# Kernel optimization log

Hardware: AMD Instinct MI355X
Metric: run time of the kernel (lower is better)

The kernel has to match this reference:

```python
import jax, jax.numpy as jnp
import numpy as np

B, U, L, H = 2048, 512, 32, 64  # batch, num_units, latent_dim, hidden


def setup_inputs() -> dict:
    key = jax.random.key(0)
    ks = jax.random.split(key, 17)
    s = 0.05  # weight scale
    inp = {
        "x": jax.random.normal(ks[0], (B, U), dtype=jnp.float32),
        # encoder: U -> 64 -> 64 -> 64 -> L
        "We1": jax.random.normal(ks[1], (U, H), jnp.float32) * s,
        "be1": jnp.zeros((H,), jnp.float32),
        "We2": jax.random.normal(ks[2], (H, H), jnp.float32) * s,
        "be2": jnp.zeros((H,), jnp.float32),
        "We3": jax.random.normal(ks[3], (H, H), jnp.float32) * s,
        "be3": jnp.zeros((H,), jnp.float32),
        "We4": jax.random.normal(ks[4], (H, L), jnp.float32) * s,
        "be4": jnp.zeros((L,), jnp.float32),
        # U disjoint decoders, weights stacked along unit axis: L -> 64 -> 64 -> 64 -> 1
        "Wd1": jax.random.normal(ks[5], (U, L, H), jnp.float32) * s,
        "bd1": jnp.zeros((U, H), jnp.float32),
        "Wd2": jax.random.normal(ks[6], (U, H, H), jnp.float32) * s,
        "bd2": jnp.zeros((U, H), jnp.float32),
        "Wd3": jax.random.normal(ks[7], (U, H, H), jnp.float32) * s,
        "bd3": jnp.zeros((U, H), jnp.float32),
        "Wd4": jax.random.normal(ks[8], (U, H), jnp.float32) * s,  # last layer out_dim=1, squeezed
        "bd4": jnp.zeros((U,), jnp.float32),
    }
    return inp


def reference(x, We1, be1, We2, be2, We3, be3, We4, be4,
              Wd1, bd1, Wd2, bd2, Wd3, bd3, Wd4, bd4):
    # shared encoder MLP: [B, U] -> [B, L]
    z = jax.nn.relu(x @ We1 + be1)
    z = jax.nn.relu(z @ We2 + be2)
    z = jax.nn.relu(z @ We3 + be3)
    z = z @ We4 + be4  # [B, L]
    # all U decoders batched as grouped GEMMs: [B, L] -> [B, U]
    h = jax.nn.relu(jnp.einsum('bl,ulh->buh', z, Wd1) + bd1)   # [B, U, H]
    h = jax.nn.relu(jnp.einsum('buh,uhk->buk', h, Wd2) + bd2)  # [B, U, H]
    h = jax.nn.relu(jnp.einsum('buh,uhk->buk', h, Wd3) + bd3)  # [B, U, H]
    out = jnp.einsum('buh,uh->bu', h, Wd4) + bd4               # [B, U]
    return out
```

## Files before the change

kernel.cpp:

```cpp
#include <hip/hip_runtime.h>
#include <hip/hip_bf16.h>
#include <hip/hip_fp16.h>
#include <stdint.h>

#define NB 2048
#define NU 512
#define NL 32
#define NH 64

typedef float    f4    __attribute__((ext_vector_type(4)));
typedef uint32_t u32x4 __attribute__((ext_vector_type(4)));
typedef _Float16 h8    __attribute__((ext_vector_type(8)));
typedef _Float16 h2    __attribute__((ext_vector_type(2)));

__device__ __forceinline__ f4 mfma16h(u32x4 a, u32x4 b, f4 c) {
    return __builtin_amdgcn_mfma_f32_16x16x32_f16(
        __builtin_bit_cast(h8, a), __builtin_bit_cast(h8, b), c, 0, 0, 0);
}

__device__ __forceinline__ uint32_t pk2h(float a, float b) {
    uint32_t la = (uint32_t)__half_as_ushort(__float2half_rn(a));
    uint32_t hb = (uint32_t)__half_as_ushort(__float2half_rn(b));
    return la | (hb << 16);
}

__device__ __forceinline__ uint32_t pk_rtz(float e, float o) {
    return __builtin_bit_cast(uint32_t, __builtin_amdgcn_cvt_pkrtz(e, o));
}

__device__ __forceinline__ uint32_t pk_relu(float e, float o) {
    uint32_t r = pk_rtz(e, o);
    asm("v_pk_max_f16 %0, %1, 0" : "=v"(r) : "v"(r));
    return r;
}

__device__ __forceinline__ float dot2(uint32_t a, uint32_t b, float c) {
    return __builtin_amdgcn_fdot2(__builtin_bit_cast(h2, a),
                                  __builtin_bit_cast(h2, b), c, false);
}

__device__ __forceinline__ void xch(uint32_t A, uint32_t B,
                                    uint32_t& o0, uint32_t& o1) {
    asm("v_permlane32_swap_b32 %0, %1" : "+v"(A), "+v"(B));
    asm("v_permlane16_swap_b32 %0, %1" : "+v"(A), "+v"(B));
    o0 = A; o1 = B;
}

__global__ __launch_bounds__(256)
void enc_kernel(const float* __restrict__ x,
                const float* __restrict__ We1, const float* __restrict__ be1,
                const float* __restrict__ We2, const float* __restrict__ be2,
                const float* __restrict__ We3, const float* __restrict__ be3,
                const float* __restrict__ We4, const float* __restrict__ be4,
                uint32_t* __restrict__ zpk)
{
    const int RE = 8;
    __shared__ float xs[RE][512];
    __shared__ float ws[128 * 64];
    __shared__ float h[RE][NH];
    __shared__ float h2s[RE][NH];

    const int t  = threadIdx.x;
    const int r0 = blockIdx.x * RE;

    {
        const f4* xv  = (const f4*)(x + (size_t)r0 * 512);
        f4*       xsv = (f4*)&xs[0][0];
        for (int i = t; i < RE * 512 / 4; i += 256) xsv[i] = xv[i];
    }

    const int j = t & 63;
    const int w = t >> 6;

    float acc0 = be1[j], acc1 = be1[j];
    for (int kc = 0; kc < 512; kc += 128) {
        __syncthreads();
        const f4* wv  = (const f4*)(We1 + (size_t)kc * 64);
        f4*       wsv = (f4*)ws;
        for (int i = t; i < 128 * 64 / 4; i += 256) wsv[i] = wv[i];
        __syncthreads();
        #pragma unroll 8
        for (int k = 0; k < 128; ++k) {
            float wval = ws[k * 64 + j];
            acc0 = fmaf(xs[w][kc + k],     wval, acc0);
            acc1 = fmaf(xs[w + 4][kc + k], wval, acc1);
        }
    }
    acc0 = fmaxf(acc0, 0.f); acc1 = fmaxf(acc1, 0.f);
    __syncthreads();
    h[w][j] = acc0; h[w + 4][j] = acc1;
    __syncthreads();

    acc0 = be2[j]; acc1 = be2[j];
    #pragma unroll
    for (int k = 0; k < 64; ++k) {
        float wval = We2[k * 64 + j];
        acc0 = fmaf(h[w][k],     wval, acc0);
        acc1 = fmaf(h[w + 4][k], wval, acc1);
    }
    acc0 = fmaxf(acc0, 0.f); acc1 = fmaxf(acc1, 0.f);
    h2s[w][j] = acc0; h2s[w + 4][j] = acc1;
    __syncthreads();

    acc0 = be3[j]; acc1 = be3[j];
    #pragma unroll
    for (int k = 0; k < 64; ++k) {
        float wval = We3[k * 64 + j];
        acc0 = fmaf(h2s[w][k],     wval, acc0);
        acc1 = fmaf(h2s[w + 4][k], wval, acc1);
    }
    acc0 = fmaxf(acc0, 0.f); acc1 = fmaxf(acc1, 0.f);
    h[w][j] = acc0; h[w + 4][j] = acc1;
    __syncthreads();

    const int j4  = t & 31;
    const int row = t >> 5;
    float acc = be4[j4];
    #pragma unroll
    for (int k = 0; k < 64; ++k)
        acc = fmaf(h[row][k], We4[k * 32 + j4], acc);
    float nb = __shfl_xor(acc, 1);
    if ((j4 & 1) == 0)
        zpk[(size_t)(r0 + row) * 16 + (j4 >> 1)] = pk2h(acc, nb);
}

template <int K2>
__device__ __forceinline__ void stageW(const float* __restrict__ g,
                                       uint32_t (*dst)[68], int t)
{
    for (int g4 = t; g4 < K2 * 16; g4 += 256) {
        const int k2 = g4 >> 4, c4 = (g4 & 15) << 2;
        f4 a = *(const f4*)(g + (size_t)(2 * k2) * NH + c4);
        f4 b = *(const f4*)(g + (size_t)(2 * k2 + 1) * NH + c4);
        u32x4 p;
        p[0] = pk2h(a[0], b[0]);
        p[1] = pk2h(a[1], b[1]);
        p[2] = pk2h(a[2], b[2]);
        p[3] = pk2h(a[3], b[3]);
        *(u32x4*)&dst[k2][c4] = p;
    }
}

__global__ __launch_bounds__(256)
void dec_kernel(const uint32_t* __restrict__ zpk,
                const float* __restrict__ Wd1, const float* __restrict__ bd1,
                const float* __restrict__ Wd2, const float* __restrict__ bd2,
                const float* __restrict__ Wd3, const float* __restrict__ bd3,
                const float* __restrict__ Wd4, const float* __restrict__ bd4,
                float* __restrict__ out)
{
    __shared__ uint32_t wpk1[16][68];
    __shared__ uint32_t wpk2[32][68];
    __shared__ uint32_t wpk3[150][68];
    __shared__ float bsh[3][NH];
    __shared__ float w4s[NH];

    const int bid = blockIdx.x;
    const int u = ((bid & 7) << 4) | (((bid >> 3) & 3) << 7) | (bid >> 5);
    const int t = threadIdx.x;

    stageW<16>(Wd1 + (size_t)u * NL * NH, wpk1, t);
    stageW<32>(Wd2 + (size_t)u * NH * NH, wpk2, t);
    stageW<32>(Wd3 + (size_t)u * NH * NH, wpk3, t);
    if (t < NH) {
        bsh[0][t] = bd1[(size_t)u * NH + t];
        bsh[1][t] = bd2[(size_t)u * NH + t];
        bsh[2][t] = bd3[(size_t)u * NH + t];
        w4s[t]    = Wd4[(size_t)u * NH + t];
    }
    __syncthreads();

    const int w  = t >> 6;
    const int lr = t & 15;
    const int lg = (t & 63) >> 4;
    const float b4 = bd4[u];

    u32x4 a1[4], a2[4][2], a3[4][2];
    #pragma unroll
    for (int mt = 0; mt < 4; ++mt) {
        const int c = lr + 16 * mt;
        #pragma unroll
        for (int i = 0; i < 4; ++i)
            a1[mt][i] = wpk1[lg * 4 + i][c];
        #pragma unroll
        for (int ks = 0; ks < 2; ++ks) {
            #pragma unroll
            for (int i = 0; i < 4; ++i) {
                a2[mt][ks][i] = wpk2[ks * 16 + lg * 4 + i][c];
                a3[mt][ks][i] = wpk3[ks * 16 + lg * 4 + i][c];
            }
        }
    }

    f4 bc1[4], bc2[4], bc3[4];
    #pragma unroll
    for (int mt = 0; mt < 4; ++mt) {
        bc1[mt] = *(const f4*)&bsh[0][16 * mt + lg * 4];
        bc2[mt] = *(const f4*)&bsh[1][16 * mt + lg * 4];
        bc3[mt] = *(const f4*)&bsh[2][16 * mt + lg * 4];
    }

    uint32_t wd4pk[4][2];
    #pragma unroll
    for (int mt = 0; mt < 4; ++mt) {
        const int c = 16 * mt + lg * 4;
        wd4pk[mt][0] = pk2h(w4s[c],     w4s[c + 1]);
        wd4pk[mt][1] = pk2h(w4s[c + 2], w4s[c + 3]);
    }

    const int rl = w * 16 + lr;

    u32x4 zc[2];
    zc[0] = *(const u32x4*)(zpk + (size_t)rl * 16 + lg * 4);
    zc[1] = *(const u32x4*)(zpk + (size_t)(64 + rl) * 16 + lg * 4);

    for (int it = 0; it < 16; ++it) {
        const int rb    = it * 128 + rl;
        const int rbn   = ((it + 1) & 15) * 128 + rl;
        u32x4 zn[2];
        zn[0] = *(const u32x4*)(zpk + (size_t)rbn * 16 + lg * 4);
        zn[1] = *(const u32x4*)(zpk + (size_t)(rbn + 64) * 16 + lg * 4);

        f4 acc[2][4];
        uint32_t pk1_[2][4][2], pk2_[2][4][2];

        #pragma unroll
        for (int s = 0; s < 2; ++s)
            #pragma unroll
            for (int mt = 0; mt < 4; ++mt)
                acc[s][mt] = mfma16h(a1[mt], zc[s], bc1[mt]);

        #pragma unroll
        for (int s = 0; s < 2; ++s)
            #pragma unroll
            for (int mt = 0; mt < 4; ++mt) {
                pk1_[s][mt][0] = pk_relu(acc[s][mt][0], acc[s][mt][1]);
                pk1_[s][mt][1] = pk_relu(acc[s][mt][2], acc[s][mt][3]);
            }

        #pragma unroll
        for (int s = 0; s < 2; ++s) {
            u32x4 bf;
            uint32_t b0, b2, b1, b3;
            xch(pk1_[s][0][0], pk1_[s][1][0], b0, b2);
            xch(pk1_[s][0][1], pk1_[s][1][1], b1, b3);
            bf[0] = b0; bf[1] = b1; bf[2] = b2; bf[3] = b3;
            #pragma unroll
            for (int mt = 0; mt < 4; ++mt)
                acc[s][mt] = mfma16h(a2[mt][0], bf, bc2[mt]);
        }
        #pragma unroll
        for (int s = 0; s < 2; ++s) {
            u32x4 bf;
            uint32_t b0, b2, b1, b3;
            xch(pk1_[s][2][0], pk1_[s][3][0], b0, b2);
            xch(pk1_[s][2][1], pk1_[s][3][1], b1, b3);
            bf[0] = b0; bf[1] = b1; bf[2] = b2; bf[3] = b3;
            #pragma unroll
            for (int mt = 0; mt < 4; ++mt)
                acc[s][mt] = mfma16h(a2[mt][1], bf, acc[s][mt]);
        }

        #pragma unroll
        for (int s = 0; s < 2; ++s)
            #pragma unroll
            for (int mt = 0; mt < 4; ++mt) {
                pk2_[s][mt][0] = pk_relu(acc[s][mt][0], acc[s][mt][1]);
                pk2_[s][mt][1] = pk_relu(acc[s][mt][2], acc[s][mt][3]);
            }

        #pragma unroll
        for (int s = 0; s < 2; ++s) {
            u32x4 bf;
            uint32_t b0, b2, b1, b3;
            xch(pk2_[s][0][0], pk2_[s][1][0], b0, b2);
            xch(pk2_[s][0][1], pk2_[s][1][1], b1, b3);
            bf[0] = b0; bf[1] = b1; bf[2] = b2; bf[3] = b3;
            #pragma unroll
            for (int mt = 0; mt < 4; ++mt)
                acc[s][mt] = mfma16h(a3[mt][0], bf, bc3[mt]);
        }
        #pragma unroll
        for (int s = 0; s < 2; ++s) {
            u32x4 bf;
            uint32_t b0, b2, b1, b3;
            xch(pk2_[s][2][0], pk2_[s][3][0], b0, b2);
            xch(pk2_[s][2][1], pk2_[s][3][1], b1, b3);
            bf[0] = b0; bf[1] = b1; bf[2] = b2; bf[3] = b3;
            #pragma unroll
            for (int mt = 0; mt < 4; ++mt)
                acc[s][mt] = mfma16h(a3[mt][1], bf, acc[s][mt]);
        }

        float part[2] = {0.f, 0.f};
        #pragma unroll
        for (int s = 0; s < 2; ++s)
            #pragma unroll
            for (int mt = 0; mt < 4; ++mt) {
                uint32_t p0 = pk_relu(acc[s][mt][0], acc[s][mt][1]);
                uint32_t p1 = pk_relu(acc[s][mt][2], acc[s][mt][3]);
                part[s] = dot2(p0, wd4pk[mt][0], part[s]);
                part[s] = dot2(p1, wd4pk[mt][1], part[s]);
            }
        #pragma unroll
        for (int s = 0; s < 2; ++s) {
            part[s] += __shfl_xor(part[s], 16);
            part[s] += __shfl_xor(part[s], 32);
        }
        if ((t & 48) == 0) {
            out[(size_t)rb * NU + u]        = part[0] + b4;
            out[(size_t)(rb + 64) * NU + u] = part[1] + b4;
        }

        zc[0] = zn[0]; zc[1] = zn[1];
    }
}

extern "C" void kernel_launch(void* const* d_in, const int* in_sizes, int n_in,
                              void* d_out, int out_size, void* d_ws, size_t ws_size,
                              hipStream_t stream)
{
    const float* x   = (const float*)d_in[0];
    const float* We1 = (const float*)d_in[1];
    const float* be1 = (const float*)d_in[2];
    const float* We2 = (const float*)d_in[3];
    const float* be2 = (const float*)d_in[4];
    const float* We3 = (const float*)d_in[5];
    const float* be3 = (const float*)d_in[6];
    const float* We4 = (const float*)d_in[7];
    const float* be4 = (const float*)d_in[8];
    const float* Wd1 = (const float*)d_in[9];
    const float* bd1 = (const float*)d_in[10];
    const float* Wd2 = (const float*)d_in[11];
    const float* bd2 = (const float*)d_in[12];
    const float* Wd3 = (const float*)d_in[13];
    const float* bd3 = (const float*)d_in[14];
    const float* Wd4 = (const float*)d_in[15];
    const float* bd4 = (const float*)d_in[16];
    float* out = (float*)d_out;

    uint32_t* zpk = (uint32_t*)d_ws;

    enc_kernel<<<NB / 8, 256, 0, stream>>>(x, We1, be1, We2, be2, We3, be3,
                                           We4, be4, zpk);
    dec_kernel<<<NU, 256, 0, stream>>>(zpk, Wd1, bd1, Wd2, bd2,
                                       Wd3, bd3, Wd4, bd4, out);
}
```

Baseline: 52.30 us.

## Permute hidden-unit ordering in weight fragments to eliminate cross-lane permlane swaps

Reorders which hidden columns each MFMA M-tile produces (cperm/bq mapping) so that each layer's packed ReLU output already sits in the lane layout the next MFMA needs as its B operand. This removes the permlane32/permlane16 swap instructions between layers. Biases and the final-layer weights are remapped to match. The final dot product is also split into two independent accumulators to shorten the dependency chain.

```diff
diff --git a/kernel.cpp b/kernel.cpp
--- a/kernel.cpp
+++ b/kernel.cpp
@@ -37,13 +37,6 @@
 __device__ __forceinline__ float dot2(uint32_t a, uint32_t b, float c) {
     return __builtin_amdgcn_fdot2(__builtin_bit_cast(h2, a),
                                   __builtin_bit_cast(h2, b), c, false);
-}
-
-__device__ __forceinline__ void xch(uint32_t A, uint32_t B,
-                                    uint32_t& o0, uint32_t& o1) {
-    asm("v_permlane32_swap_b32 %0, %1" : "+v"(A), "+v"(B));
-    asm("v_permlane16_swap_b32 %0, %1" : "+v"(A), "+v"(B));
-    o0 = A; o1 = B;
 }
 
 __global__ __launch_bounds__(256)
@@ -175,10 +168,15 @@
     const int lg = (t & 63) >> 4;
     const float b4 = bd4[u];
 
+    int cperm[4];
+    #pragma unroll
+    for (int mt = 0; mt < 4; ++mt)
+        cperm[mt] = ((mt >> 1) << 5) + ((lr >> 2) << 3) + ((mt & 1) << 2) + (lr & 3);
+
     u32x4 a1[4], a2[4][2], a3[4][2];
     #pragma unroll
     for (int mt = 0; mt < 4; ++mt) {
-        const int c = lr + 16 * mt;
+        const int c = cperm[mt];
         #pragma unroll
         for (int i = 0; i < 4; ++i)
             a1[mt][i] = wpk1[lg * 4 + i][c];
@@ -192,20 +190,24 @@
         }
     }
 
+    int bq[4];
+    #pragma unroll
+    for (int mt = 0; mt < 4; ++mt)
+        bq[mt] = ((mt >> 1) << 5) + (lg << 3) + ((mt & 1) << 2);
+
     f4 bc1[4], bc2[4], bc3[4];
     #pragma unroll
     for (int mt = 0; mt < 4; ++mt) {
-        bc1[mt] = *(const f4*)&bsh[0][16 * mt + lg * 4];
-        bc2[mt] = *(const f4*)&bsh[1][16 * mt + lg * 4];
-        bc3[mt] = *(const f4*)&bsh[2][16 * mt + lg * 4];
+        bc1[mt] = *(const f4*)&bsh[0][bq[mt]];
+        bc2[mt] = *(const f4*)&bsh[1][bq[mt]];
+        bc3[mt] = *(const f4*)&bsh[2][bq[mt]];
     }
 
     uint32_t wd4pk[4][2];
     #pragma unroll
     for (int mt = 0; mt < 4; ++mt) {
-        const int c = 16 * mt + lg * 4;
-        wd4pk[mt][0] = pk2h(w4s[c],     w4s[c + 1]);
-        wd4pk[mt][1] = pk2h(w4s[c + 2], w4s[c + 3]);
+        wd4pk[mt][0] = pk2h(w4s[bq[mt]],     w4s[bq[mt] + 1]);
+        wd4pk[mt][1] = pk2h(w4s[bq[mt] + 2], w4s[bq[mt] + 3]);
     }
 
     const int rl = w * 16 + lr;
@@ -215,14 +217,13 @@
     zc[1] = *(const u32x4*)(zpk + (size_t)(64 + rl) * 16 + lg * 4);
 
     for (int it = 0; it < 16; ++it) {
-        const int rb    = it * 128 + rl;
-        const int rbn   = ((it + 1) & 15) * 128 + rl;
+        const int rb  = it * 128 + rl;
+        const int rbn = ((it + 1) & 15) * 128 + rl;
         u32x4 zn[2];
         zn[0] = *(const u32x4*)(zpk + (size_t)rbn * 16 + lg * 4);
         zn[1] = *(const u32x4*)(zpk + (size_t)(rbn + 64) * 16 + lg * 4);
 
         f4 acc[2][4];
-        uint32_t pk1_[2][4][2], pk2_[2][4][2];
 
         #pragma unroll
         for (int s = 0; s < 2; ++s)
@@ -230,86 +231,68 @@
             for (int mt = 0; mt < 4; ++mt)
                 acc[s][mt] = mfma16h(a1[mt], zc[s], bc1[mt]);
 
-        #pragma unroll
-        for (int s = 0; s < 2; ++s)
-            #pragma unroll
-            for (int mt = 0; mt < 4; ++mt) {
-                pk1_[s][mt][0] = pk_relu(acc[s][mt][0], acc[s][mt][1]);
-                pk1_[s][mt][1] = pk_relu(acc[s][mt][2], acc[s][mt][3]);
-            }
-
+        u32x4 bf0[2], bf1[2];
         #pragma unroll
         for (int s = 0; s < 2; ++s) {
-            u32x4 bf;
-            uint32_t b0, b2, b1, b3;
-            xch(pk1_[s][0][0], pk1_[s][1][0], b0, b2);
-            xch(pk1_[s][0][1], pk1_[s][1][1], b1, b3);
-            bf[0] = b0; bf[1] = b1; bf[2] = b2; bf[3] = b3;
-            #pragma unroll
-            for (int mt = 0; mt < 4; ++mt)
-                acc[s][mt] = mfma16h(a2[mt][0], bf, bc2[mt]);
-        }
+            bf0[s][0] = pk_relu(acc[s][0][0], acc[s][0][1]);
+            bf0[s][1] = pk_relu(acc[s][0][2], acc[s][0][3]);
+            bf0[s][2] = pk_relu(acc[s][1][0], acc[s][1][1]);
+            bf0[s][3] = pk_relu(acc[s][1][2], acc[s][1][3]);
+            bf1[s][0] = pk_relu(acc[s][2][0], acc[s][2][1]);
+            bf1[s][1] = pk_relu(acc[s][2][2], acc[s][2][3]);
+            bf1[s][2] = pk_relu(acc[s][3][0], acc[s][3][1]);
+            bf1[s][3] = pk_relu(acc[s][3][2], acc[s][3][3]);
+        }
+
+        #pragma unroll
+        for (int s = 0; s < 2; ++s)
+            #pragma unroll
+            for (int mt = 0; mt < 4; ++mt)
+                acc[s][mt] = mfma16h(a2[mt][0], bf0[s], bc2[mt]);
+        #pragma unroll
+        for (int s = 0; s < 2; ++s)
+            #pragma unroll
+            for (int mt = 0; mt < 4; ++mt)
+                acc[s][mt] = mfma16h(a2[mt][1], bf1[s], acc[s][mt]);
+
         #pragma unroll
         for (int s = 0; s < 2; ++s) {
-            u32x4 bf;
-            uint32_t b0, b2, b1, b3;
-            xch(pk1_[s][2][0], pk1_[s][3][0], b0, b2);
-            xch(pk1_[s][2][1], pk1_[s][3][1], b1, b3);
-            bf[0] = b0; bf[1] = b1; bf[2] = b2; bf[3] = b3;
-            #pragma unroll
-            for (int mt = 0; mt < 4; ++mt)
-                acc[s][mt] = mfma16h(a2[mt][1], bf, acc[s][mt]);
-        }
-
-        #pragma unroll
-        for (int s = 0; s < 2; ++s)
-            #pragma unroll
-            for (int mt = 0; mt < 4; ++mt) {
-                pk2_[s][mt][0] = pk_relu(acc[s][mt][0], acc[s][mt][1]);
-                pk2_[s][mt][1] = pk_relu(acc[s][mt][2], acc[s][mt][3]);
-            }
+            bf0[s][0] = pk_relu(acc[s][0][0], acc[s][0][1]);
+            bf0[s][1] = pk_relu(acc[s][0][2], acc[s][0][3]);
+            bf0[s][2] = pk_relu(acc[s][1][0], acc[s][1][1]);
+            bf0[s][3] = pk_relu(acc[s][1][2], acc[s][1][3]);
+            bf1[s][0] = pk_relu(acc[s][2][0], acc[s][2][1]);
+            bf1[s][1] = pk_relu(acc[s][2][2], acc[s][2][3]);
+            bf1[s][2] = pk_relu(acc[s][3][0], acc[s][3][1]);
+            bf1[s][3] = pk_relu(acc[s][3][2], acc[s][3][3]);
+        }
+
+        #pragma unroll
+        for (int s = 0; s < 2; ++s)
+            #pragma unroll
+            for (int mt = 0; mt < 4; ++mt)
+                acc[s][mt] = mfma16h(a3[mt][0], bf0[s], bc3[mt]);
+        #pragma unroll
+        for (int s = 0; s < 2; ++s)
+            #pragma unroll
+            for (int mt = 0; mt < 4; ++mt)
+                acc[s][mt] = mfma16h(a3[mt][1], bf1[s], acc[s][mt]);
 
         #pragma unroll
         for (int s = 0; s < 2; ++s) {
-            u32x4 bf;
-            uint32_t b0, b2, b1, b3;
-            xch(pk2_[s][0][0], pk2_[s][1][0], b0, b2);
-            xch(pk2_[s][0][1], pk2_[s][1][1], b1, b3);
-            bf[0] = b0; bf[1] = b1; bf[2] = b2; bf[3] = b3;
-            #pragma unroll
-            for (int mt = 0; mt < 4; ++mt)
-                acc[s][mt] = mfma16h(a3[mt][0], bf, bc3[mt]);
-        }
-        #pragma unroll
-        for (int s = 0; s < 2; ++s) {
-            u32x4 bf;
-            uint32_t b0, b2, b1, b3;
-            xch(pk2_[s][2][0], pk2_[s][3][0], b0, b2);
-            xch(pk2_[s][2][1], pk2_[s][3][1], b1, b3);
-            bf[0] = b0; bf[1] = b1; bf[2] = b2; bf[3] = b3;
-            #pragma unroll
-            for (int mt = 0; mt < 4; ++mt)
-                acc[s][mt] = mfma16h(a3[mt][1], bf, acc[s][mt]);
-        }
-
-        float part[2] = {0.f, 0.f};
-        #pragma unroll
-        for (int s = 0; s < 2; ++s)
+            float pa = 0.f, pb = 0.f;
             #pragma unroll
             for (int mt = 0; mt < 4; ++mt) {
                 uint32_t p0 = pk_relu(acc[s][mt][0], acc[s][mt][1]);
                 uint32_t p1 = pk_relu(acc[s][mt][2], acc[s][mt][3]);
-                part[s] = dot2(p0, wd4pk[mt][0], part[s]);
-                part[s] = dot2(p1, wd4pk[mt][1], part[s]);
+                pa = dot2(p0, wd4pk[mt][0], pa);
+                pb = dot2(p1, wd4pk[mt][1], pb);
             }
-        #pragma unroll
-        for (int s = 0; s < 2; ++s) {
-            part[s] += __shfl_xor(part[s], 16);
-            part[s] += __shfl_xor(part[s], 32);
-        }
-        if ((t & 48) == 0) {
-            out[(size_t)rb * NU + u]        = part[0] + b4;
-            out[(size_t)(rb + 64) * NU + u] = part[1] + b4;
+            float part = pa + pb;
+            part += __shfl_xor(part, 16);
+            part += __shfl_xor(part, 32);
+            if ((t & 48) == 0)
+                out[(size_t)(rb + s * 64) * NU + u] = part + b4;
         }
 
         zc[0] = zn[0]; zc[1] = zn[1];
```

After: 48.30 us. 1.08x faster.
